# Performance work log

Hardware: AMD Instinct MI355X
Metric: run time of the kernel (lower is better)

The kernel has to match this reference:

```python
import jax, jax.numpy as jnp
from jax import lax
import numpy as np

WS = 8        # window size
SHIFT = 4     # shift size
HEADS = 4
EPS = 1e-5


def _rel_pos_index(ws):
    coords = np.stack(np.meshgrid(np.arange(ws), np.arange(ws), indexing='ij'))  # (2,ws,ws)
    cf = coords.reshape(2, -1)
    rel = cf[:, :, None] - cf[:, None, :]           # (2,n,n)
    rel = rel.transpose(1, 2, 0).astype(np.int64)   # (n,n,2)
    rel[:, :, 0] += ws - 1
    rel[:, :, 1] += ws - 1
    rel[:, :, 0] *= 2 * ws - 1
    return rel.sum(-1)                              # (n,n)


def _attn_mask(h, w, ws, ss):
    img = np.zeros((h, w), dtype=np.float32)
    cnt = 0
    for hs in (slice(0, -ws), slice(-ws, -ss), slice(-ss, None)):
        for wsl in (slice(0, -ws), slice(-ws, -ss), slice(-ss, None)):
            img[hs, wsl] = cnt
            cnt += 1
    mw = img.reshape(h // ws, ws, w // ws, ws).transpose(0, 2, 1, 3).reshape(-1, ws * ws)
    am = mw[:, None, :] - mw[:, :, None]            # (nW,n,n)
    return np.where(am != 0, -100.0, 0.0).astype(np.float32)


def _ln(x, w, b):
    mu = x.mean(-1, keepdims=True)
    var = jnp.var(x, axis=-1, keepdims=True)
    return (x - mu) * lax.rsqrt(var + EPS) * w + b


def setup_inputs() -> dict:
    key = jax.random.key(0)
    ks = jax.random.split(key, 16)
    b, c, h, w = 4, 64, 256, 256
    hidden = 4 * c
    n_bias = (2 * WS - 1) * (2 * WS - 1)
    s = 0.02
    return {
        'x': jax.random.normal(ks[0], (b, c, h, w), jnp.float32),
        'norm1_w': jnp.ones((c,), jnp.float32),
        'norm1_b': jnp.zeros((c,), jnp.float32),
        'qkv_w': jax.random.normal(ks[1], (3 * c, c), jnp.float32) * s,
        'qkv_b': jnp.zeros((3 * c,), jnp.float32),
        'rpb': jax.random.normal(ks[2], (n_bias, HEADS), jnp.float32) * s,
        'proj_w': jax.random.normal(ks[3], (c, c), jnp.float32) * s,
        'proj_b': jnp.zeros((c,), jnp.float32),
        'norm2_w': jnp.ones((c,), jnp.float32),
        'norm2_b': jnp.zeros((c,), jnp.float32),
        'fc1_w': jax.random.normal(ks[4], (hidden, c), jnp.float32) * s,
        'fc1_b': jnp.zeros((hidden,), jnp.float32),
        'dw_w': jax.random.normal(ks[5], (hidden, 1, 5, 5), jnp.float32) * s,
        'dw_b': jnp.zeros((hidden,), jnp.float32),
        'fc2_w': jax.random.normal(ks[6], (c, hidden), jnp.float32) * s,
        'fc2_b': jnp.zeros((c,), jnp.float32),
    }


def reference(x, norm1_w, norm1_b, qkv_w, qkv_b, rpb, proj_w, proj_b,
              norm2_w, norm2_b, fc1_w, fc1_b, dw_w, dw_b, fc2_w, fc2_b):
    b, c, h, w = x.shape
    d = c // HEADS
    scale = d ** (-0.5)
    n = WS * WS

    x3 = jnp.transpose(x.reshape(b, c, h * w), (0, 2, 1))  # (b, hw, c)
    shortcut = x3
    xn = _ln(x3, norm1_w, norm1_b).reshape(b, h, w, c)

    # cyclic shift + window partition
    sx = jnp.roll(xn, (-SHIFT, -SHIFT), axis=(1, 2))
    win = sx.reshape(b, h // WS, WS, w // WS, WS, c).transpose(0, 1, 3, 2, 4, 5).reshape(-1, n, c)
    B_ = win.shape[0]

    qkv = (win @ qkv_w.T + qkv_b).reshape(B_, n, 3, HEADS, d).transpose(2, 0, 3, 1, 4)
    q, k, v = qkv[0] * scale, qkv[1], qkv[2]   # (B_, H, n, d)
    attn = jnp.einsum('bhnd,bhmd->bhnm', q, k)  # (B_, H, n, n)

    bias = rpb[jnp.asarray(_rel_pos_index(WS)).reshape(-1)].reshape(n, n, HEADS).transpose(2, 0, 1)
    attn = attn + bias[None]

    mask = jnp.asarray(_attn_mask(h, w, WS, SHIFT))  # (nW, n, n)
    nW = mask.shape[0]
    attn = attn.reshape(B_ // nW, nW, HEADS, n, n) + mask[None, :, None]
    attn = jax.nn.softmax(attn.reshape(B_, HEADS, n, n), axis=-1)

    out = jnp.einsum('bhnm,bhmd->bhnd', attn, v).transpose(0, 2, 1, 3).reshape(B_, n, c)
    out = out @ proj_w.T + proj_b

    # window reverse + un-shift
    sx = out.reshape(b, h // WS, w // WS, WS, WS, c).transpose(0, 1, 3, 2, 4, 5).reshape(b, h, w, c)
    xr = jnp.roll(sx, (SHIFT, SHIFT), axis=(1, 2)).reshape(b, h * w, c)
    x3 = shortcut + xr

    # ConvFFN
    xn = _ln(x3, norm2_w, norm2_b)
    hid = jax.nn.gelu(xn @ fc1_w.T + fc1_b, approximate=False)  # (b, hw, hidden)
    hidden = hid.shape[-1]
    himg = hid.transpose(0, 2, 1).reshape(b, hidden, h, w)
    dc = lax.conv_general_dilated(himg, dw_w, (1, 1), [(2, 2), (2, 2)],
                                  dimension_numbers=('NCHW', 'OIHW', 'NCHW'),
                                  feature_group_count=hidden)
    dc = jax.nn.gelu(dc + dw_b[None, :, None, None], approximate=False)
    hid = hid + dc.reshape(b, hidden, h * w).transpose(0, 2, 1)
    x3 = x3 + (hid @ fc2_w.T + fc2_b)

    return jnp.transpose(x3, (0, 2, 1)).reshape(b, c, h, w)
```

## Files before the change

### kernel.cpp

```cpp
#include <hip/hip_runtime.h>
#include <hip/hip_bf16.h>
#include <hip/hip_fp8.h>
#include <math.h>


typedef __bf16  bf16x8  __attribute__((ext_vector_type(8)));
typedef float   f32x4   __attribute__((ext_vector_type(4)));
typedef float   f32x2   __attribute__((ext_vector_type(2)));
typedef unsigned short ushortx8 __attribute__((ext_vector_type(8)));

__device__ __forceinline__ float gelu_f(float v) {
    float u = v * fmaf(0.0713548354f, v * v, 1.5957691216f);
    float t = __expf(u);
    float r = __builtin_amdgcn_rcpf(t + 1.0f);
    return v - v * r;
}
__device__ __forceinline__ unsigned char f32_to_fp8(float v) {
    __hip_fp8_e4m3 t(v);
    return (unsigned char)t.__x;
}
__device__ __forceinline__ float fp8_to_f32(unsigned char u) {
    __hip_fp8_e4m3 t;
    t.__x = (__hip_fp8_storage_t)u;
    return (float)t;
}

#if __has_builtin(__builtin_amdgcn_cvt_pk_f32_fp8) && __has_builtin(__builtin_amdgcn_cvt_pk_fp8_f32)
#define HW_FP8 1
#endif
template<bool HI>
__device__ __forceinline__ f32x2 fp8x2_f32(unsigned int u) {
#ifdef HW_FP8
    return __builtin_amdgcn_cvt_pk_f32_fp8((int)u, HI);
#else
    f32x2 r;
    const int s = HI ? 16 : 0;
    r.x = fp8_to_f32((unsigned char)(u >> s));
    r.y = fp8_to_f32((unsigned char)(u >> (s + 8)));
    return r;
#endif
}
template<bool HI>
__device__ __forceinline__ unsigned int f32x2_fp8(float a, float b, unsigned int old) {
#ifdef HW_FP8
    return (unsigned int)__builtin_amdgcn_cvt_pk_fp8_f32(a, b, (int)old, HI);
#else
    unsigned int v = (unsigned int)f32_to_fp8(a) | ((unsigned int)f32_to_fp8(b) << 8);
    return HI ? ((old & 0x0000ffffu) | (v << 16)) : ((old & 0xffff0000u) | v);
#endif
}

__device__ __forceinline__ unsigned short f2bf(float f) {
    unsigned int u = __builtin_bit_cast(unsigned int, f);
    u += 0x7fffu + ((u >> 16) & 1u);
    return (unsigned short)(u >> 16);
}
__device__ __forceinline__ float bf2f(unsigned short u) {
    return __builtin_bit_cast(float, ((unsigned int)u) << 16);
}

__global__ __launch_bounds__(256) void k_prep(
        const float* __restrict__ qkvw, const float* __restrict__ projw,
        const float* __restrict__ rpb,  const float* __restrict__ fc1w,
        unsigned short* __restrict__ qkvw_bf, unsigned short* __restrict__ projw_bf,
        unsigned short* __restrict__ rpb_bf,  unsigned short* __restrict__ fc1w_bf) {
    const int i = blockIdx.x * 256 + threadIdx.x;
    if (i < 12288) qkvw_bf[i] = f2bf(qkvw[i]);
    if (i < 4096)  projw_bf[i] = f2bf(projw[i]);
    if (i < 900)   rpb_bf[i]   = f2bf(rpb[i]);
    if (i < 16384) fc1w_bf[i]  = f2bf(fc1w[i]);
}

__global__ __launch_bounds__(256) void k_cvt(const float* __restrict__ src,
        unsigned short* __restrict__ dst, int n) {
    const int i = blockIdx.x * 256 + threadIdx.x;
    if (i < n) dst[i] = f2bf(src[i]);
}

__global__ __launch_bounds__(256) void k_ln1(const float* __restrict__ x,
        const float* __restrict__ w1, const float* __restrict__ b1,
        unsigned short* __restrict__ A, unsigned short* __restrict__ Bw) {
    __shared__ float tile[64 * 65];
    __shared__ float red0[256], red1[256];
    __shared__ float muv[64], rsv[64], lw[64], lb[64];
    const int tid = threadIdx.x;
    const int gid = blockIdx.x;
    const int xc = gid & 3, y = (gid >> 2) & 255, b = gid >> 10;
    const int x0 = xc * 64;
    if (tid < 64) { lw[tid] = w1[tid]; lb[tid] = b1[tid]; }

    const float* xb = x + ((size_t)b * 64) * 65536 + y * 256 + x0;
    {
        const int tk = tid & 63, cl = tid >> 6;
        for (int it = 0; it < 16; ++it) {
            int cc = cl + 4 * it;
            tile[cc * 65 + tk] = xb[(size_t)cc * 65536 + tk];
        }
    }
    __syncthreads();
    {
        const int tk = tid & 63, cl = tid >> 6;
        float s = 0.f, s2 = 0.f;
        #pragma unroll
        for (int k = 0; k < 16; ++k) {
            float v = tile[(cl * 16 + k) * 65 + tk];
            s += v; s2 += v * v;
        }
        red0[cl * 64 + tk] = s; red1[cl * 64 + tk] = s2;
    }
    __syncthreads();
    if (tid < 64) {
        float s  = red0[tid] + red0[64 + tid] + red0[128 + tid] + red0[192 + tid];
        float s2 = red1[tid] + red1[64 + tid] + red1[128 + tid] + red1[192 + tid];
        float mu = s * (1.f / 64.f);
        float var = s2 * (1.f / 64.f) - mu * mu;
        muv[tid] = mu; rsv[tid] = rsqrtf(var + 1e-5f);
    }
    __syncthreads();
    const int ch = tid & 63, tl = tid >> 6;
    const int ys = (y + 252) & 255;
    const int wy = ys >> 3, py = ys & 7;
    for (int it = 0; it < 16; ++it) {
        int t = tl + 4 * it;
        float v = tile[ch * 65 + t];
        int tok = (b << 16) + y * 256 + x0 + t;
        A[(size_t)tok * 64 + ch] = f2bf(v);
        float vn = (v - muv[t]) * rsv[t] * lw[ch] + lb[ch];
        int xs = (x0 + t + 252) & 255;
        int wx = xs >> 3, px = xs & 7;
        int widx = (b << 10) + (wy << 5) + wx;
        int pos = (py << 3) + px;
        Bw[((size_t)widx * 64 + pos) * 64 + ch] = f2bf(vn);
    }
}

__global__ __launch_bounds__(256) void k_attn(
        const unsigned short* __restrict__ Bw,
        const unsigned short* __restrict__ qkvw_bf,
        const unsigned short* __restrict__ projw_bf,
        const unsigned short* __restrict__ rpb_bf,
        const float* __restrict__ qkvb,
        const float* __restrict__ projb,
        const unsigned short* __restrict__ A, unsigned short* __restrict__ Cb) {
    __shared__ __align__(16) unsigned short Xs[4608];
    __shared__ __align__(16) unsigned short Ws[13824];
    __shared__ __align__(8)  unsigned short rpbl[900];
    __shared__ float qkvbl[192];
    __shared__ float projbl[64];

    const int tid = threadIdx.x;
    const int lane = tid & 63, wv = tid >> 6;
    const int l15 = lane & 15, quad = lane >> 4;
    const int widx = blockIdx.x;
    const int wib = widx & 1023;
    const int wy = wib >> 5, wx = wib & 31, bimg = widx >> 10;
    const bool edge = (wy == 31) | (wx == 31);

    const f32x4 zz = {0.f, 0.f, 0.f, 0.f};
    const ushortx8 zu = {0, 0, 0, 0, 0, 0, 0, 0};
    const bf16x8 z8 = __builtin_bit_cast(bf16x8, zu);

    const ushortx8 pw0 = *(const ushortx8*)(projw_bf + tid * 8);
    const ushortx8 pw1 = *(const ushortx8*)(projw_bf + (256 + tid) * 8);

    {
        const unsigned short* Xg = Bw + (size_t)widx * 4096 + wv * 1024;
        #pragma unroll
        for (int it = 0; it < 2; ++it) {
            int g = it * 64 + lane;
            int row = g >> 3, c8 = g & 7;
            *(ushortx8*)&Xs[(wv * 16 + row) * 72 + c8 * 8] =
                *(const ushortx8*)(Xg + g * 8);
        }
    }
    #pragma unroll
    for (int it = 0; it < 6; ++it) {
        int g = it * 256 + tid;
        int row = g >> 3, c8 = g & 7;
        *(ushortx8*)&Ws[row * 72 + c8 * 8] = *(const ushortx8*)(qkvw_bf + g * 8);
    }
    if (tid < 225) *(uint2*)&rpbl[tid * 4] = *(const uint2*)(rpb_bf + tid * 4);
    if (tid < 192) qkvbl[tid] = qkvb[tid];
    if (tid < 64)  projbl[tid] = projb[tid];
    __syncthreads();

    f32x4 qacc[12];
    #pragma unroll
    for (int i = 0; i < 12; ++i) qacc[i] = zz;
    {
        const bf16x8 av0 = *(const bf16x8*)&Xs[(16 * wv + l15) * 72 + quad * 8];
        const bf16x8 av1 = *(const bf16x8*)&Xs[(16 * wv + l15) * 72 + 32 + quad * 8];
        #pragma unroll
        for (int gl = 0; gl < 12; ++gl) {
            bf16x8 bv0 = *(const bf16x8*)&Ws[(gl * 16 + l15) * 72 + quad * 8];
            qacc[gl] = __builtin_amdgcn_mfma_f32_16x16x32_bf16(av0, bv0, qacc[gl], 0, 0, 0);
            bf16x8 bv1 = *(const bf16x8*)&Ws[(gl * 16 + l15) * 72 + 32 + quad * 8];
            qacc[gl] = __builtin_amdgcn_mfma_f32_16x16x32_bf16(av1, bv1, qacc[gl], 0, 0, 0);
        }
    }
    __syncthreads();

    #pragma unroll
    for (int g = 0; g < 12; ++g) {
        #pragma unroll
        for (int r = 0; r < 4; ++r) {
            int tok = 16 * wv + quad * 4 + r;
            int oc  = g * 16 + l15;
            float v = qacc[g][r] + qkvbl[oc];
            if (g < 4)       Ws[g * 1024 + tok * 16 + l15] = f2bf(v * 0.25f);
            else if (g < 8)  Ws[4096 + (g - 4) * 1024 + tok * 16 + l15] = f2bf(v);
            else             Ws[8192 + ((g - 8) * 16 + l15) * 72 + tok] = f2bf(v);
        }
    }
    __syncthreads();

    f32x4 sacc[4][4];
    #pragma unroll
    for (int h = 0; h < 4; ++h) {
        bf16x8 qa = z8;
        if (quad < 2) qa = *(const bf16x8*)&Ws[h * 1024 + (16 * wv + l15) * 16 + quad * 8];
        #pragma unroll
        for (int nt = 0; nt < 4; ++nt) {
            bf16x8 kf = z8;
            if (quad < 2) kf = *(const bf16x8*)&Ws[4096 + h * 1024 + (nt * 16 + l15) * 16 + quad * 8];
            sacc[h][nt] = __builtin_amdgcn_mfma_f32_16x16x32_bf16(qa, kf, zz, 0, 0, 0);
        }
    }
    __syncthreads();

    {
        const int r0 = tid >> 3;
        *(ushortx8*)&Ws[4096 + r0 * 64 + (((tid & 7) ^ (r0 & 7)) << 3)] = pw0;
        const int g1 = 256 + tid, r1 = g1 >> 3;
        *(ushortx8*)&Ws[4096 + r1 * 64 + (((g1 & 7) ^ (r1 & 7)) << 3)] = pw1;
    }

    const int jhi = l15 >> 3, jlo = l15 & 7;
    int offj4[4], regj[4];
    #pragma unroll
    for (int nt = 0; nt < 4; ++nt) {
        int j = nt * 16 + l15;
        int jy = j >> 3, jx = j & 7;
        offj4[nt] = (jy * 15 + jx) * 4;
        regj[nt] = 0;
        if (edge) {
            int ysj = wy * 8 + jy, xsj = wx * 8 + jx;
            regj[nt] = (ysj >= 252 ? 2 : (ysj >= 248 ? 1 : 0)) * 3
                     + (xsj >= 252 ? 2 : (xsj >= 248 ? 1 : 0));
        }
    }
    int rbA[4], regiA[4], pbaseA[4], i7A[4];
    #pragma unroll
    for (int r = 0; r < 4; ++r) {
        const int i = 16 * wv + quad * 4 + r;
        const int iy = i >> 3, ix = i & 7;
        rbA[r] = ((iy + 7) * 15 + (ix + 7)) * 4;
        i7A[r] = i & 7;
        pbaseA[r] = i * 64 + jlo;
        regiA[r] = 0;
        if (edge) {
            const int ysi = wy * 8 + iy, xsi = wx * 8 + ix;
            regiA[r] = (ysi >= 252 ? 2 : (ysi >= 248 ? 1 : 0)) * 3
                     + (xsi >= 252 ? 2 : (xsi >= 248 ? 1 : 0));
        }
    }

    f32x4 o[4];
    #pragma unroll
    for (int h = 0; h < 4; ++h) {
        float invh[4];
        #pragma unroll
        for (int r = 0; r < 4; ++r) {
            float m0 = -1e30f;
            #pragma unroll
            for (int nt = 0; nt < 4; ++nt) {
                float s = sacc[h][nt][r] + bf2f(rpbl[rbA[r] + h - offj4[nt]]);
                if (edge) s += (regj[nt] == regiA[r]) ? 0.f : -100.f;
                sacc[h][nt][r] = s;
                m0 = fmaxf(m0, s);
            }
            m0 = fmaxf(m0, __shfl_xor(m0, 1));
            m0 = fmaxf(m0, __shfl_xor(m0, 2));
            m0 = fmaxf(m0, __shfl_xor(m0, 4));
            m0 = fmaxf(m0, __shfl_xor(m0, 8));
            float s0 = 0.f;
            #pragma unroll
            for (int nt = 0; nt < 4; ++nt) {
                float e = __expf(sacc[h][nt][r] - m0);
                s0 += e;
                Ws[pbaseA[r] + ((((nt << 1) | jhi) ^ i7A[r]) << 3)] = f2bf(e);
            }
            s0 += __shfl_xor(s0, 1); s0 += __shfl_xor(s0, 2);
            s0 += __shfl_xor(s0, 4); s0 += __shfl_xor(s0, 8);
            invh[r] = 1.f / s0;
        }
        o[h] = zz;
        #pragma unroll
        for (int s = 0; s < 2; ++s) {
            bf16x8 pa = *(const bf16x8*)&Ws[(16 * wv + l15) * 64
                                            + (((s * 4 + quad) ^ (l15 & 7)) << 3)];
            bf16x8 vb = *(const bf16x8*)&Ws[8192 + (h * 16 + l15) * 72 + s * 32 + quad * 8];
            o[h] = __builtin_amdgcn_mfma_f32_16x16x32_bf16(pa, vb, o[h], 0, 0, 0);
        }
        #pragma unroll
        for (int r = 0; r < 4; ++r) o[h][r] *= invh[r];
    }

    unsigned short resid[16];
    #pragma unroll
    for (int r = 0; r < 4; ++r) {
        int tok = 16 * wv + quad * 4 + r;
        int py = tok >> 3, px = tok & 7;
        int yo = (wy * 8 + py + 4) & 255, xo = (wx * 8 + px + 4) & 255;
        size_t gt = ((size_t)bimg << 16) + yo * 256 + xo;
        #pragma unroll
        for (int nt = 0; nt < 4; ++nt)
            resid[r * 4 + nt] = A[gt * 64 + nt * 16 + l15];
    }

    #pragma unroll
    for (int h = 0; h < 4; ++h)
        #pragma unroll
        for (int r = 0; r < 4; ++r)
            Xs[(16 * wv + quad * 4 + r) * 72 + h * 16 + l15] = f2bf(o[h][r]);
    __syncthreads();

    f32x4 pacc[4];
    #pragma unroll
    for (int nt = 0; nt < 4; ++nt) {
        pacc[nt] = zz;
        #pragma unroll
        for (int s = 0; s < 2; ++s) {
            bf16x8 oa = *(const bf16x8*)&Xs[(16 * wv + l15) * 72 + s * 32 + quad * 8];
            bf16x8 wb = *(const bf16x8*)&Ws[4096 + (nt * 16 + l15) * 64
                                            + (((s * 4 + quad) ^ (l15 & 7)) << 3)];
            pacc[nt] = __builtin_amdgcn_mfma_f32_16x16x32_bf16(oa, wb, pacc[nt], 0, 0, 0);
        }
    }

    #pragma unroll
    for (int r = 0; r < 4; ++r) {
        int tok = 16 * wv + quad * 4 + r;
        int py = tok >> 3, px = tok & 7;
        int yo = (wy * 8 + py + 4) & 255, xo = (wx * 8 + px + 4) & 255;
        size_t gt = ((size_t)bimg << 16) + yo * 256 + xo;
        #pragma unroll
        for (int nt = 0; nt < 4; ++nt) {
            int oc = nt * 16 + l15;
            float v = pacc[nt][r] + projbl[oc] + bf2f(resid[r * 4 + nt]);
            Cb[gt * 64 + oc] = f2bf(v);
        }
    }
}

__global__ __launch_bounds__(256) void k_ln2fc1(const unsigned short* __restrict__ Cb,
        const float* __restrict__ w2, const float* __restrict__ b2,
        const unsigned short* __restrict__ fc1w_bf, const float* __restrict__ fc1b,
        unsigned char* __restrict__ D) {
    __shared__ __align__(16) unsigned short Xb[64 * 72];
    __shared__ __align__(16) unsigned short Wb[256 * 72];
    __shared__ float red0[256], red1[256];
    __shared__ float muv[64], rsv[64], lwv[64], lbv[64], fb[256];
    const int tid = threadIdx.x, gid = blockIdx.x;
    const int xc = gid & 3, y = (gid >> 2) & 255, b = gid >> 10;
    const int x0 = xc * 64;
    const int lane = tid & 63, wv = tid >> 6;
    const int l15 = lane & 15, quad = lane >> 4;
    const f32x4 zz = {0.f, 0.f, 0.f, 0.f};

    if (tid < 64) { lwv[tid] = w2[tid]; lbv[tid] = b2[tid]; }
    fb[tid] = fc1b[tid];

    const unsigned short* Cp = Cb + ((size_t)(b << 16) + y * 256 + x0) * 64;
    #pragma unroll
    for (int it = 0; it < 16; ++it) {
        int tt = wv + 4 * it;
        Xb[tt * 72 + lane] = Cp[tt * 64 + lane];
    }
    {
        const ushortx8* w8 = (const ushortx8*)fc1w_bf;
        #pragma unroll
        for (int it = 0; it < 8; ++it) {
            int idx = it * 256 + tid;
            int row = idx >> 3, c8 = idx & 7;
            *(ushortx8*)&Wb[row * 72 + c8 * 8] = w8[idx];
        }
    }
    __syncthreads();
    {
        const int tok = tid & 63, cl = tid >> 6;
        float s = 0.f, s2 = 0.f;
        #pragma unroll
        for (int g = 0; g < 2; ++g) {
            const ushortx8 u = *(const ushortx8*)&Xb[tok * 72 + cl * 16 + g * 8];
            #pragma unroll
            for (int k = 0; k < 8; ++k) { float v = bf2f(u[k]); s += v; s2 += v * v; }
        }
        red0[cl * 64 + tok] = s; red1[cl * 64 + tok] = s2;
    }
    __syncthreads();
    if (tid < 64) {
        float s  = red0[tid] + red0[64 + tid] + red0[128 + tid] + red0[192 + tid];
        float s2 = red1[tid] + red1[64 + tid] + red1[128 + tid] + red1[192 + tid];
        float mu = s * (1.f / 64.f);
        float var = s2 * (1.f / 64.f) - mu * mu;
        muv[tid] = mu; rsv[tid] = rsqrtf(var + 1e-5f);
    }
    __syncthreads();
    #pragma unroll
    for (int it = 0; it < 16; ++it) {
        int tt = wv + 4 * it;
        float v = bf2f(Xb[tt * 72 + lane]);
        v = (v - muv[tt]) * rsv[tt] * lwv[lane] + lbv[lane];
        Xb[tt * 72 + lane] = f2bf(v);
    }
    __syncthreads();

    f32x4 acc[4][4];
    #pragma unroll
    for (int mt = 0; mt < 4; ++mt)
        #pragma unroll
        for (int nt = 0; nt < 4; ++nt) acc[mt][nt] = zz;
    #pragma unroll
    for (int s = 0; s < 2; ++s) {
        bf16x8 Bf[4];
        #pragma unroll
        for (int nt = 0; nt < 4; ++nt)
            Bf[nt] = *(const bf16x8*)&Xb[(nt * 16 + l15) * 72 + s * 32 + quad * 8];
        #pragma unroll
        for (int mt = 0; mt < 4; ++mt) {
            bf16x8 Af = *(const bf16x8*)&Wb[(64 * wv + 16 * mt + l15) * 72 + s * 32 + quad * 8];
            #pragma unroll
            for (int nt = 0; nt < 4; ++nt)
                acc[mt][nt] = __builtin_amdgcn_mfma_f32_16x16x32_bf16(Af, Bf[nt], acc[mt][nt], 0, 0, 0);
        }
    }

    #pragma unroll
    for (int mt = 0; mt < 4; ++mt) {
        #pragma unroll
        for (int r = 0; r < 4; ++r) {
            const int mch = 64 * wv + 16 * mt + quad * 4 + r;
            const float bias = fb[mch];
            unsigned char* Dp = D + (((size_t)(b * 256 + mch)) << 16) + y * 256 + x0;
            float g0 = gelu_f(acc[mt][0][r] + bias);
            float g1 = gelu_f(acc[mt][1][r] + bias);
            float g2 = gelu_f(acc[mt][2][r] + bias);
            float g3 = gelu_f(acc[mt][3][r] + bias);
            unsigned int pk = f32x2_fp8<false>(g0, g1, 0u);
            pk = f32x2_fp8<true>(g2, g3, pk);
            Dp[l15]      = (unsigned char)(pk);
            Dp[16 + l15] = (unsigned char)(pk >> 8);
            Dp[32 + l15] = (unsigned char)(pk >> 16);
            Dp[48 + l15] = (unsigned char)(pk >> 24);
        }
    }
}

__global__ __launch_bounds__(256) void k_dwconv(const unsigned char* __restrict__ D,
        const float* __restrict__ dww, const float* __restrict__ dwb,
        unsigned char* __restrict__ E) {
    __shared__ __align__(16) unsigned short inT[36 * 280 + 16];
    __shared__ __align__(16) unsigned short Atab[5 * 64 * 8];
    __shared__ __align__(16) unsigned char outT[4][16 * 144];
    const int tid = threadIdx.x, gid = blockIdx.x;
    const int yt = gid & 7, pc = gid >> 3;
    const int ch = pc & 255;
    const int y0 = yt * 32;
    const unsigned char* Dp = D + ((size_t)pc << 16);
    const f32x4 zz = {0.f, 0.f, 0.f, 0.f};

    #pragma unroll
    for (int it = 0; it < 5; ++it) {
        int idx = it * 256 + tid;
        if (idx < 1262) ((uint4*)inT)[idx] = make_uint4(0, 0, 0, 0);
    }
    __syncthreads();

    #pragma unroll
    for (int it = 0; it < 9; ++it) {
        const int u = it * 256 + tid;
        const int t = u >> 6, c = u & 63;
        const int gy = y0 - 2 + t;
        if ((unsigned)gy < 256u) {
            const unsigned int v = *(const unsigned int*)(Dp + gy * 256 + 4 * c);
            const f32x2 lo = fp8x2_f32<false>(v);
            const f32x2 hi = fp8x2_f32<true>(v);
            unsigned int b01 = (unsigned)f2bf(lo.x) | ((unsigned)f2bf(lo.y) << 16);
            unsigned int b23 = (unsigned)f2bf(hi.x) | ((unsigned)f2bf(hi.y) << 16);
            unsigned int* base = (unsigned int*)&inT[t * 280 + 2 + 4 * c];
            base[0] = b01; base[1] = b23;
        }
    }
    #pragma unroll
    for (int q = 0; q < 10; ++q) {
        const int e = tid * 10 + q;
        const int ky = e >> 9, r = e & 511;
        const int l = r >> 3, j = r & 7;
        const int m = l & 15, k = ((l >> 4) << 3) + j;
        const int d = k - m;
        float wv = 0.f;
        if (d >= 0 && d < 5) wv = dww[ch * 25 + ky * 5 + d];
        Atab[e] = f2bf(wv);
    }
    const float bb = dwb[ch];
    __syncthreads();

    const int wv_ = tid >> 6, lane = tid & 63;
    const int l15 = lane & 15, quad = lane >> 4;
    const int g = wv_ >> 1, xh = wv_ & 1;
    bf16x8 Af[5];
    #pragma unroll
    for (int ky = 0; ky < 5; ++ky)
        Af[ky] = *(const bf16x8*)&Atab[(ky * 64 + lane) * 8];
    const int tbase = g * 16 + l15;

    #pragma unroll
    for (int xp = 0; xp < 8; ++xp) {
        const int xs = xh * 128 + xp * 16;
        f32x4 acc = zz;
        #pragma unroll
        for (int ky = 0; ky < 5; ++ky) {
            bf16x8 Bf = *(const bf16x8*)&inT[(tbase + ky) * 280 + xs + quad * 8];
            acc = __builtin_amdgcn_mfma_f32_16x16x32_bf16(Af[ky], Bf, acc, 0, 0, 0);
        }
        const unsigned int* cp32 = (const unsigned int*)&inT[(tbase + 2) * 280 + 2 + xs + quad * 4];
        const unsigned int c01 = cp32[0], c23 = cp32[1];
        const float c0 = bf2f((unsigned short)c01), c1 = bf2f((unsigned short)(c01 >> 16));
        const float c2 = bf2f((unsigned short)c23), c3 = bf2f((unsigned short)(c23 >> 16));
        unsigned int pk = f32x2_fp8<false>(c0 + gelu_f(acc[0] + bb), c1 + gelu_f(acc[1] + bb), 0u);
        pk = f32x2_fp8<true>(c2 + gelu_f(acc[2] + bb), c3 + gelu_f(acc[3] + bb), pk);
        *(unsigned int*)&outT[wv_][l15 * 144 + xp * 16 + quad * 4] = pk;
    }

    {
        const int row = lane >> 2, sg = lane & 3;
        unsigned char* Ep = E + ((size_t)pc << 16) + (y0 + g * 16 + row) * 256 + xh * 128 + sg * 32;
        *(uint4*)Ep        = *(const uint4*)&outT[wv_][row * 144 + sg * 32];
        *(uint4*)(Ep + 16) = *(const uint4*)&outT[wv_][row * 144 + sg * 32 + 16];
    }
}

__global__ __launch_bounds__(256) void k_fc2(const unsigned char* __restrict__ E,
        const unsigned short* __restrict__ Cb, const unsigned short* __restrict__ fc2w_bf,
        const float* __restrict__ fc2b, float* __restrict__ out) {
    __shared__ __align__(16) unsigned short Hb[64 * 136];
    __shared__ __align__(16) unsigned short Wb2[64 * 264];
    __shared__ __align__(16) unsigned short Cl[64 * 72];
    __shared__ float fbl[64];
    const int tid = threadIdx.x, gid = blockIdx.x;
    const int xc = gid & 3, y = (gid >> 2) & 255, b = gid >> 10;
    const int x0 = xc * 64;
    const int lane = tid & 63, wv = tid >> 6;
    const int l15 = lane & 15, quad = lane >> 4;
    const f32x4 zz = {0.f, 0.f, 0.f, 0.f};

    if (tid < 64) fbl[tid] = fc2b[tid];
    {
        const unsigned short* Cp = Cb + ((size_t)(b << 16) + y * 256 + x0) * 64;
        #pragma unroll
        for (int it = 0; it < 16; ++it) {
            int tt = wv + 4 * it;
            Cl[tt * 72 + lane] = Cp[tt * 64 + lane];
        }
    }
    {
        const ushortx8* w8 = (const ushortx8*)fc2w_bf;
        #pragma unroll
        for (int it = 0; it < 8; ++it) {
            int idx = it * 256 + tid;
            int row = idx >> 5, c8 = idx & 31;
            *(ushortx8*)&Wb2[row * 264 + c8 * 8] = w8[idx];
        }
    }

    f32x4 acc[4];
    #pragma unroll
    for (int nt = 0; nt < 4; ++nt) acc[nt] = zz;

    const int ldc = tid >> 4;
    const int tq  = tid & 15;
    unsigned int u0[8];
    #pragma unroll
    for (int it = 0; it < 8; ++it) {
        int chl = ldc + 16 * it;
        u0[it] = *(const unsigned int*)&E[(((size_t)(b * 256 + chl)) << 16) + y * 256 + x0 + 4 * tq];
    }
    __syncthreads();

    for (int kc = 0; kc < 2; ++kc) {
        #pragma unroll
        for (int it = 0; it < 8; ++it) {
            int chl = ldc + 16 * it;
            f32x2 lo = fp8x2_f32<false>(u0[it]);
            f32x2 hi = fp8x2_f32<true>(u0[it]);
            float vals[4] = {lo.x, lo.y, hi.x, hi.y};
            #pragma unroll
            for (int j = 0; j < 4; ++j) {
                int tok = 4 * tq + j;
                int p = (((chl >> 3) ^ (tok >> 2)) << 3) + (chl & 7);
                Hb[tok * 136 + p] = f2bf(vals[j]);
            }
        }
        if (kc == 0) {
            #pragma unroll
            for (int it = 0; it < 8; ++it) {
                int chl = ldc + 16 * it + 128;
                u0[it] = *(const unsigned int*)&E[(((size_t)(b * 256 + chl)) << 16) + y * 256 + x0 + 4 * tq];
            }
        }
        __syncthreads();
        #pragma unroll
        for (int k32 = 0; k32 < 4; ++k32) {
            bf16x8 Af = *(const bf16x8*)&Wb2[(16 * wv + l15) * 264 + kc * 128 + k32 * 32 + quad * 8];
            const int g = k32 * 4 + quad;
            #pragma unroll
            for (int nt = 0; nt < 4; ++nt) {
                const int tok = nt * 16 + l15;
                bf16x8 Bf = *(const bf16x8*)&Hb[tok * 136 + ((g ^ (tok >> 2)) << 3)];
                acc[nt] = __builtin_amdgcn_mfma_f32_16x16x32_bf16(Af, Bf, acc[nt], 0, 0, 0);
            }
        }
        if (kc == 0) __syncthreads();
    }

    #pragma unroll
    for (int r = 0; r < 4; ++r) {
        const int oc = 16 * wv + quad * 4 + r;
        const float bias = fbl[oc];
        float* op = out + (((size_t)(b * 64 + oc)) << 16) + y * 256 + x0;
        #pragma unroll
        for (int nt = 0; nt < 4; ++nt) {
            const int tok = nt * 16 + l15;
            op[tok] = acc[nt][r] + bias + bf2f(Cl[tok * 72 + oc]);
        }
    }
}

extern "C" void kernel_launch(void* const* d_in, const int* in_sizes, int n_in,
                              void* d_out, int out_size, void* d_ws, size_t ws_size,
                              hipStream_t stream) {
    const float* x     = (const float*)d_in[0];
    const float* n1w   = (const float*)d_in[1];
    const float* n1b   = (const float*)d_in[2];
    const float* qkvw  = (const float*)d_in[3];
    const float* qkvb  = (const float*)d_in[4];
    const float* rpb   = (const float*)d_in[5];
    const float* projw = (const float*)d_in[6];
    const float* projb = (const float*)d_in[7];
    const float* n2w   = (const float*)d_in[8];
    const float* n2b   = (const float*)d_in[9];
    const float* fc1w  = (const float*)d_in[10];
    const float* fc1b  = (const float*)d_in[11];
    const float* dww   = (const float*)d_in[12];
    const float* dwb   = (const float*)d_in[13];
    const float* fc2w  = (const float*)d_in[14];
    const float* fc2b  = (const float*)d_in[15];
    float* out = (float*)d_out;

    char* ws = (char*)d_ws;
    const size_t MB = 1048576;
    unsigned short* Cbuf = (unsigned short*)ws;
    unsigned short* Ab   = (unsigned short*)(ws + 32 * MB);
    unsigned short* Bwp  = (unsigned short*)(ws + 64 * MB);
    unsigned char*  Dh   = (unsigned char*)(ws + 32 * MB);
    unsigned char*  Eh   = (unsigned char*)(ws + 96 * MB);

    unsigned short* qkvw_bf = (unsigned short*)(ws + 96 * MB);
    unsigned short* projw_bf = (unsigned short*)(ws + 96 * MB + 24576);
    unsigned short* rpb_bf   = (unsigned short*)(ws + 96 * MB + 32768);
    unsigned short* fc1w_bf  = (unsigned short*)(ws + 96 * MB + 34816);
    unsigned short* fc2w_bf  = (unsigned short*)(ws + 32 * MB);

    k_prep  <<<64,    256, 0, stream>>>(qkvw, projw, rpb, fc1w,
                                        qkvw_bf, projw_bf, rpb_bf, fc1w_bf);
    k_ln1   <<<4096,  256, 0, stream>>>(x, n1w, n1b, Ab, Bwp);
    k_attn  <<<4096,  256, 0, stream>>>(Bwp, qkvw_bf, projw_bf, rpb_bf,
                                        qkvb, projb, Ab, Cbuf);
    k_ln2fc1<<<4096,  256, 0, stream>>>(Cbuf, n2w, n2b, fc1w_bf, fc1b, Dh);
    k_dwconv<<<8192,  256, 0, stream>>>(Dh, dww, dwb, Eh);
    k_cvt   <<<64,    256, 0, stream>>>(fc2w, fc2w_bf, 16384);
    k_fc2   <<<4096,  256, 0, stream>>>(Eh, Cbuf, fc2w_bf, fc2b, out);
}
```

Baseline: 389.4 us.

## Drop softmax max-subtraction, compute row sums via MFMA, vectorize bias loads

The softmax in the window-attention kernel no longer computes a per-row max with cross-lane shuffles and no longer subtracts it before exponentiating. The row sums now come from an extra MFMA against a ones matrix instead of shuffle reductions, and are inverted with a fast reciprocal. The relative-position bias for all four heads is read with one 8-byte LDS load and added in a separate pre-pass. Exponentials are packed to bf16 with the gfx950 pack-convert instruction. The aim is to cut shuffle and VALU work in the softmax, but without max-subtraction large scores could overflow, and the bf16 row sum is less precise.

```diff
diff --git a/kernel.cpp b/kernel.cpp
--- a/kernel.cpp
+++ b/kernel.cpp
@@ -58,6 +58,15 @@
 __device__ __forceinline__ float bf2f(unsigned short u) {
     return __builtin_bit_cast(float, ((unsigned int)u) << 16);
 }
+__device__ __forceinline__ unsigned int cvt_pk_bf16(float a, float b) {
+#if defined(__gfx950__)
+    unsigned int r;
+    asm("v_cvt_pk_bf16_f32 %0, %1, %2" : "=v"(r) : "v"(a), "v"(b));
+    return r;
+#else
+    return (unsigned int)f2bf(a) | ((unsigned int)f2bf(b) << 16);
+#endif
+}
 
 __global__ __launch_bounds__(256) void k_prep(
         const float* __restrict__ qkvw, const float* __restrict__ projw,
@@ -159,6 +168,8 @@
     const f32x4 zz = {0.f, 0.f, 0.f, 0.f};
     const ushortx8 zu = {0, 0, 0, 0, 0, 0, 0, 0};
     const bf16x8 z8 = __builtin_bit_cast(bf16x8, zu);
+    const ushortx8 ou = {0x3F80, 0x3F80, 0x3F80, 0x3F80, 0x3F80, 0x3F80, 0x3F80, 0x3F80};
+    const bf16x8 ones8 = __builtin_bit_cast(bf16x8, ou);
 
     const ushortx8 pw0 = *(const ushortx8*)(projw_bf + tid * 8);
     const ushortx8 pw1 = *(const ushortx8*)(projw_bf + (256 + tid) * 8);
@@ -265,45 +276,52 @@
         }
     }
 
+    #pragma unroll
+    for (int r = 0; r < 4; ++r) {
+        #pragma unroll
+        for (int nt = 0; nt < 4; ++nt) {
+            const uint2 bw = *(const uint2*)&rpbl[rbA[r] - offj4[nt]];
+            float mk = 0.f;
+            if (edge) mk = (regj[nt] == regiA[r]) ? 0.f : -100.f;
+            sacc[0][nt][r] += __builtin_bit_cast(float, bw.x << 16) + mk;
+            sacc[1][nt][r] += __builtin_bit_cast(float, bw.x & 0xffff0000u) + mk;
+            sacc[2][nt][r] += __builtin_bit_cast(float, bw.y << 16) + mk;
+            sacc[3][nt][r] += __builtin_bit_cast(float, bw.y & 0xffff0000u) + mk;
+        }
+    }
+    int pA_[4][4];
+    #pragma unroll
+    for (int r = 0; r < 4; ++r)
+        #pragma unroll
+        for (int nt = 0; nt < 4; ++nt)
+            pA_[r][nt] = pbaseA[r] + ((((nt << 1) | jhi) ^ i7A[r]) << 3);
+
     f32x4 o[4];
     #pragma unroll
     for (int h = 0; h < 4; ++h) {
-        float invh[4];
         #pragma unroll
         for (int r = 0; r < 4; ++r) {
-            float m0 = -1e30f;
-            #pragma unroll
-            for (int nt = 0; nt < 4; ++nt) {
-                float s = sacc[h][nt][r] + bf2f(rpbl[rbA[r] + h - offj4[nt]]);
-                if (edge) s += (regj[nt] == regiA[r]) ? 0.f : -100.f;
-                sacc[h][nt][r] = s;
-                m0 = fmaxf(m0, s);
-            }
-            m0 = fmaxf(m0, __shfl_xor(m0, 1));
-            m0 = fmaxf(m0, __shfl_xor(m0, 2));
-            m0 = fmaxf(m0, __shfl_xor(m0, 4));
-            m0 = fmaxf(m0, __shfl_xor(m0, 8));
-            float s0 = 0.f;
-            #pragma unroll
-            for (int nt = 0; nt < 4; ++nt) {
-                float e = __expf(sacc[h][nt][r] - m0);
-                s0 += e;
-                Ws[pbaseA[r] + ((((nt << 1) | jhi) ^ i7A[r]) << 3)] = f2bf(e);
-            }
-            s0 += __shfl_xor(s0, 1); s0 += __shfl_xor(s0, 2);
-            s0 += __shfl_xor(s0, 4); s0 += __shfl_xor(s0, 8);
-            invh[r] = 1.f / s0;
+            const unsigned int pk01 = cvt_pk_bf16(__expf(sacc[h][0][r]),
+                                                  __expf(sacc[h][1][r]));
+            const unsigned int pk23 = cvt_pk_bf16(__expf(sacc[h][2][r]),
+                                                  __expf(sacc[h][3][r]));
+            Ws[pA_[r][0]] = (unsigned short)pk01;
+            Ws[pA_[r][1]] = (unsigned short)(pk01 >> 16);
+            Ws[pA_[r][2]] = (unsigned short)pk23;
+            Ws[pA_[r][3]] = (unsigned short)(pk23 >> 16);
         }
         o[h] = zz;
+        f32x4 os = zz;
         #pragma unroll
         for (int s = 0; s < 2; ++s) {
             bf16x8 pa = *(const bf16x8*)&Ws[(16 * wv + l15) * 64
                                             + (((s * 4 + quad) ^ (l15 & 7)) << 3)];
             bf16x8 vb = *(const bf16x8*)&Ws[8192 + (h * 16 + l15) * 72 + s * 32 + quad * 8];
             o[h] = __builtin_amdgcn_mfma_f32_16x16x32_bf16(pa, vb, o[h], 0, 0, 0);
-        }
-        #pragma unroll
-        for (int r = 0; r < 4; ++r) o[h][r] *= invh[r];
+            os   = __builtin_amdgcn_mfma_f32_16x16x32_bf16(pa, ones8, os, 0, 0, 0);
+        }
+        #pragma unroll
+        for (int r = 0; r < 4; ++r) o[h][r] *= __builtin_amdgcn_rcpf(os[r]);
     }
 
     unsigned short resid[16];
```

New measurement: 361.7 us. -7.1%, faster.
